# Optimization experiments

Hardware: AMD Instinct MI355X
Metric: run time of the kernel (lower is better)

## Reference

```python
import jax, jax.numpy as jnp
import numpy as np

POOL = 7  # fixed 7x7 output grid, hard-coded in the original layer


def _bin_bounds(step, rlen):
    # Replicates the original bin-corner logic + empty-bin adjustment.
    i = jnp.arange(POOL, dtype=jnp.int32)
    s = i * step
    e = jnp.where(i < POOL - 1, (i + 1) * step, rlen)
    empty = s == e
    # original: grow end by 1 if room, else shrink start by 1
    e = jnp.where(empty & (e < rlen), e + 1, e)
    s = jnp.where(empty & ~(e > (i * step)) , s, s)  # no-op placeholder for clarity
    s = jnp.where(empty & ((i * step) == e), (i * step) - 1, jnp.where(empty, i * step, s))
    # simpler equivalent: if still empty after trying to grow end, shrink start
    s0 = i * step
    e0 = jnp.where(i < POOL - 1, (i + 1) * step, rlen)
    grow = empty & (e0 < rlen)
    e = jnp.where(grow, e0 + 1, e0)
    s = jnp.where(empty & ~grow, s0 - 1, s0)
    return s, e


def _pool_one(roi, fm):
    # fm: [H, W, C]; roi: [4] normalized (y1, x1, y2, x2)
    H, W, C = fm.shape
    h0 = (H * roi[0]).astype(jnp.int32)  # tf.cast to int32 truncates (floor for >=0)
    w0 = (W * roi[1]).astype(jnp.int32)
    h1 = (H * roi[2]).astype(jnp.int32)
    w1 = (W * roi[3]).astype(jnp.int32)
    rh = h1 - h0
    rw = w1 - w0
    hstep = rh // POOL
    wstep = rw // POOL
    sh, eh = _bin_bounds(hstep, rh)  # [7], region-relative
    sw, ew = _bin_bounds(wstep, rw)
    hidx = jnp.arange(H, dtype=jnp.int32)
    widx = jnp.arange(W, dtype=jnp.int32)
    rmask = (hidx[None, :] >= (h0 + sh)[:, None]) & (hidx[None, :] < (h0 + eh)[:, None])  # [7,H]
    cmask = (widx[None, :] >= (w0 + sw)[:, None]) & (widx[None, :] < (w0 + ew)[:, None])  # [7,W]
    neg = jnp.asarray(-jnp.inf, fm.dtype)
    # max over rows for each of the 7 row-bins: [7, W, C]
    t = jnp.max(jnp.where(rmask[:, :, None, None], fm[None, :, :, :], neg), axis=1)
    # max over cols for each of the 7 col-bins: [7, 7, C]
    out = jnp.max(jnp.where(cmask[None, :, :, None], t[:, None, :, :], neg), axis=2)
    return out


def setup_inputs() -> dict:
    key = jax.random.key(0)
    k_f, k_y, k_x, k_h, k_w = jax.random.split(key, 5)
    H, W, C, N = 50, 50, 1024, 300
    features = jax.random.normal(k_f, (1, H, W, C), dtype=jnp.float32)
    # well-formed normalized ROIs: y1 < y2, x1 < x2, extent in [0.2, 0.55]
    y1 = jax.random.uniform(k_y, (N,), minval=0.0, maxval=0.45)
    x1 = jax.random.uniform(k_x, (N,), minval=0.0, maxval=0.45)
    hh = jax.random.uniform(k_h, (N,), minval=0.2, maxval=0.55)
    ww = jax.random.uniform(k_w, (N,), minval=0.2, maxval=0.55)
    rois = jnp.stack([y1, x1, jnp.minimum(y1 + hh, 1.0), jnp.minimum(x1 + ww, 1.0)], axis=1).astype(jnp.float32)
    return {"features": features, "rois": rois}


def reference(features, rois):
    fm = jnp.squeeze(features, axis=0)  # [H, W, C]
    # sequential over ROIs (mirrors tf.while_loop), fully vectorized per ROI
    pooled = jax.lax.map(lambda r: _pool_one(r, fm), rois)  # [N, 7, 7, C]
    return pooled
```

## Files before the change

### kernel.cpp

```cpp
#include <hip/hip_runtime.h>
#include <math.h>

#define POOL 7
#define FH 50
#define FW 50
#define FC 1024
#define FC4 (FC / 4)
#define CHUNKS 4
#define F4C 64
#define RS (FW * FC4)
#define JGROUPS 4
#define UNITS_PER_ROI (POOL * JGROUPS)
#define GRID 1024

typedef float vf4 __attribute__((ext_vector_type(4)));

static __device__ __forceinline__ vf4 vmax4(vf4 a, vf4 b) {
    vf4 r;
    r.x = fmaxf(a.x, b.x);
    r.y = fmaxf(a.y, b.y);
    r.z = fmaxf(a.z, b.z);
    r.w = fmaxf(a.w, b.w);
    return r;
}

template<int W>
static __device__ __forceinline__ void pool_w(
    const vf4* __restrict__ base,
    int r0, int nrows, int w0, int rw, int jg,
    vf4& a0, vf4& a1)
{
    if (jg < 3) {
        const int c0 = w0 + (jg * 2) * W;
        const vf4* p = base + (size_t)r0 * RS + (size_t)c0 * FC4;
        int t = 0;
        for (; t + 2 <= nrows; t += 2) {
            vf4 v0[2 * W], v1[2 * W];
#pragma unroll
            for (int k = 0; k < 2 * W; ++k) v0[k] = p[k * FC4];
#pragma unroll
            for (int k = 0; k < 2 * W; ++k) v1[k] = p[RS + k * FC4];
#pragma unroll
            for (int k = 0; k < W; ++k) a0 = vmax4(a0, vmax4(v0[k], v1[k]));
#pragma unroll
            for (int k = W; k < 2 * W; ++k) a1 = vmax4(a1, vmax4(v0[k], v1[k]));
            p += 2 * RS;
        }
        if (t < nrows) {
            vf4 v0[2 * W];
#pragma unroll
            for (int k = 0; k < 2 * W; ++k) v0[k] = p[k * FC4];
#pragma unroll
            for (int k = 0; k < W; ++k) a0 = vmax4(a0, v0[k]);
#pragma unroll
            for (int k = W; k < 2 * W; ++k) a1 = vmax4(a1, v0[k]);
        }
    } else {
        const int bw = rw - 6 * W;
        const int c0 = w0 + 6 * W;
        const vf4* p = base + (size_t)r0 * RS + (size_t)c0 * FC4;
        for (int r = 0; r < nrows; ++r) {
            vf4 v[W + 6];
#pragma unroll
            for (int k = 0; k < W + 6; ++k) {
                const int kc = (k < bw) ? k : (bw - 1);
                v[k] = p[kc * FC4];
            }
#pragma unroll
            for (int k = 0; k < W + 6; ++k) a0 = vmax4(a0, v[k]);
            p += RS;
        }
    }
}

__global__ __launch_bounds__(256, 4) void roipool_kernel(
    const float* __restrict__ fm,
    const float* __restrict__ rois,
    float* __restrict__ out,
    int nunits)
{
    const int b     = blockIdx.x;
    const int chunk = b & (CHUNKS - 1);
    const int wave  = threadIdx.x >> 6;
    const int lane  = threadIdx.x & 63;
    const int wv    = (b >> 2) * 4 + wave;

    const int f4 = chunk * F4C + lane;
    const vf4* base = reinterpret_cast<const vf4*>(fm) + f4;

    for (int u = wv; u < nunits; u += GRID) {
        const int n   = u / UNITS_PER_ROI;
        const int rem = u - n * UNITS_PER_ROI;
        const int i   = rem >> 2;
        const int jg  = rem & 3;
        const int j0  = jg * 2;
        const int jcnt = (jg < JGROUPS - 1) ? 2 : 1;

        const float4 roi = reinterpret_cast<const float4*>(rois)[n];
        const int h0 = (int)((float)FH * roi.x);
        const int w0 = (int)((float)FW * roi.y);
        const int h1 = (int)((float)FH * roi.z);
        const int w1 = (int)((float)FW * roi.w);
        const int rh = h1 - h0;
        const int rw = w1 - w0;
        const int hstep = rh / POOL;
        const int wstep = rw / POOL;

        vf4 a0 = {-INFINITY, -INFINITY, -INFINITY, -INFINITY};
        vf4 a1 = a0;

        if (hstep >= 1 && wstep >= 1 && wstep <= 3) {
            const int r0    = h0 + i * hstep;
            const int nrows = (i < POOL - 1) ? hstep : (rh - 6 * hstep);
            switch (wstep) {
                case 1: pool_w<1>(base, r0, nrows, w0, rw, jg, a0, a1); break;
                case 2: pool_w<2>(base, r0, nrows, w0, rw, jg, a0, a1); break;
                default: pool_w<3>(base, r0, nrows, w0, rw, jg, a0, a1); break;
            }
        } else {
            int sh = i * hstep;
            int eh = (i < POOL - 1) ? (i + 1) * hstep : rh;
            if (sh == eh) { if (eh < rh) eh += 1; else sh -= 1; }
            const int rr0 = max(0, h0 + sh);
            const int rr1 = min(FH, h0 + eh);

            int c0[2], c1[2];
#pragma unroll
            for (int t = 0; t < 2; ++t) {
                const int j = j0 + t;
                if (j < POOL) {
                    int sw = j * wstep;
                    int ew = (j < POOL - 1) ? (j + 1) * wstep : rw;
                    if (sw == ew) { if (ew < rw) ew += 1; else sw -= 1; }
                    c0[t] = max(0, w0 + sw);
                    c1[t] = min(FW, w0 + ew);
                } else {
                    c0[t] = 0; c1[t] = 0;
                }
            }
            for (int r = rr0; r < rr1; ++r) {
                const vf4* rowp = base + (size_t)r * RS;
#pragma unroll
                for (int t = 0; t < 2; ++t) {
                    vf4 acc = (t == 0) ? a0 : a1;
                    for (int c = c0[t]; c < c1[t]; ++c) {
                        acc = vmax4(acc, rowp[c * FC4]);
                    }
                    if (t == 0) a0 = acc; else a1 = acc;
                }
            }
        }

        vf4* o = reinterpret_cast<vf4*>(out)
               + (size_t)(n * 49 + i * 7 + j0) * FC4 + f4;
        __builtin_nontemporal_store(a0, o);
        if (jcnt == 2) {
            __builtin_nontemporal_store(a1, o + (size_t)FC4);
        }
    }
}

extern "C" void kernel_launch(void* const* d_in, const int* in_sizes, int n_in,
                              void* d_out, int out_size, void* d_ws, size_t ws_size,
                              hipStream_t stream) {
    const float* features = (const float*)d_in[0];
    const float* rois     = (const float*)d_in[1];
    float* out            = (float*)d_out;
    const int N = in_sizes[1] / 4;

    const int nunits = N * UNITS_PER_ROI;
    dim3 grid(GRID);
    dim3 block(256);
    roipool_kernel<<<grid, block, 0, stream>>>(features, rois, out, nunits);
}
```

Baseline: 102.7 us.

## Precompute 2x2/2x1/1x2 max tables to cut per-bin load count

Adds a prepass kernel that builds pairwise-max tables (vertical pair, horizontal pair, 2x2 quad) of the feature map in workspace. The pooling kernel then covers each bin with overlapping 2-strided reads from these tables, roughly halving or quartering the number of loads per bin. The cost is an extra kernel launch that reads the full feature map and writes up to three map-sized tables. The templated unrolled per-wstep paths are replaced by a generic loop.

```diff
diff --git a/kernel.cpp b/kernel.cpp
--- a/kernel.cpp
+++ b/kernel.cpp
@@ -12,6 +12,9 @@
 #define JGROUPS 4
 #define UNITS_PER_ROI (POOL * JGROUPS)
 #define GRID 1024
+#define NCELLS (FH * FW)
+#define TBL_ELEMS ((size_t)NCELLS * FC)
+#define TBL_BYTES (TBL_ELEMS * sizeof(float))
 
 typedef float vf4 __attribute__((ext_vector_type(4)));
 
@@ -24,60 +27,37 @@
     return r;
 }
 
-template<int W>
-static __device__ __forceinline__ void pool_w(
-    const vf4* __restrict__ base,
-    int r0, int nrows, int w0, int rw, int jg,
-    vf4& a0, vf4& a1)
+__global__ __launch_bounds__(256) void build_tables(
+    const float* __restrict__ fm,
+    float* __restrict__ p1, float* __restrict__ c1, float* __restrict__ q,
+    int mask)
 {
-    if (jg < 3) {
-        const int c0 = w0 + (jg * 2) * W;
-        const vf4* p = base + (size_t)r0 * RS + (size_t)c0 * FC4;
-        int t = 0;
-        for (; t + 2 <= nrows; t += 2) {
-            vf4 v0[2 * W], v1[2 * W];
-#pragma unroll
-            for (int k = 0; k < 2 * W; ++k) v0[k] = p[k * FC4];
-#pragma unroll
-            for (int k = 0; k < 2 * W; ++k) v1[k] = p[RS + k * FC4];
-#pragma unroll
-            for (int k = 0; k < W; ++k) a0 = vmax4(a0, vmax4(v0[k], v1[k]));
-#pragma unroll
-            for (int k = W; k < 2 * W; ++k) a1 = vmax4(a1, vmax4(v0[k], v1[k]));
-            p += 2 * RS;
-        }
-        if (t < nrows) {
-            vf4 v0[2 * W];
-#pragma unroll
-            for (int k = 0; k < 2 * W; ++k) v0[k] = p[k * FC4];
-#pragma unroll
-            for (int k = 0; k < W; ++k) a0 = vmax4(a0, v0[k]);
-#pragma unroll
-            for (int k = W; k < 2 * W; ++k) a1 = vmax4(a1, v0[k]);
-        }
-    } else {
-        const int bw = rw - 6 * W;
-        const int c0 = w0 + 6 * W;
-        const vf4* p = base + (size_t)r0 * RS + (size_t)c0 * FC4;
-        for (int r = 0; r < nrows; ++r) {
-            vf4 v[W + 6];
-#pragma unroll
-            for (int k = 0; k < W + 6; ++k) {
-                const int kc = (k < bw) ? k : (bw - 1);
-                v[k] = p[kc * FC4];
-            }
-#pragma unroll
-            for (int k = 0; k < W + 6; ++k) a0 = vmax4(a0, v[k]);
-            p += RS;
-        }
-    }
+    const int cell = blockIdx.x;
+    const int t    = threadIdx.x;
+    const int r    = cell / FW;
+    const int c    = cell - r * FW;
+    const int rr   = (r + 1 < FH) ? r + 1 : r;
+    const int cc   = (c + 1 < FW) ? c + 1 : c;
+
+    const vf4* fm4 = reinterpret_cast<const vf4*>(fm);
+    const size_t i00 = (size_t)cell * FC4 + t;
+    const vf4 v00 = fm4[(size_t)(r  * FW + c ) * FC4 + t];
+    const vf4 v10 = fm4[(size_t)(rr * FW + c ) * FC4 + t];
+    const vf4 v01 = fm4[(size_t)(r  * FW + cc) * FC4 + t];
+    const vf4 v11 = fm4[(size_t)(rr * FW + cc) * FC4 + t];
+
+    if (mask & 1) reinterpret_cast<vf4*>(p1)[i00] = vmax4(v00, v10);
+    if (mask & 2) reinterpret_cast<vf4*>(c1)[i00] = vmax4(v00, v01);
+    if (mask & 4) reinterpret_cast<vf4*>(q)[i00]  = vmax4(vmax4(v00, v10), vmax4(v01, v11));
 }
 
 __global__ __launch_bounds__(256, 4) void roipool_kernel(
     const float* __restrict__ fm,
     const float* __restrict__ rois,
     float* __restrict__ out,
-    int nunits)
+    int nunits,
+    const float* __restrict__ p1, const float* __restrict__ c1,
+    const float* __restrict__ q, int mask)
 {
     const int b     = blockIdx.x;
     const int chunk = b & (CHUNKS - 1);
@@ -86,7 +66,6 @@
     const int wv    = (b >> 2) * 4 + wave;
 
     const int f4 = chunk * F4C + lane;
-    const vf4* base = reinterpret_cast<const vf4*>(fm) + f4;
 
     for (int u = wv; u < nunits; u += GRID) {
         const int n   = u / UNITS_PER_ROI;
@@ -106,16 +85,44 @@
         const int hstep = rh / POOL;
         const int wstep = rw / POOL;
 
-        vf4 a0 = {-INFINITY, -INFINITY, -INFINITY, -INFINITY};
-        vf4 a1 = a0;
+        vf4* o = reinterpret_cast<vf4*>(out)
+               + (size_t)(n * 49 + i * 7 + j0) * FC4 + f4;
 
-        if (hstep >= 1 && wstep >= 1 && wstep <= 3) {
-            const int r0    = h0 + i * hstep;
-            const int nrows = (i < POOL - 1) ? hstep : (rh - 6 * hstep);
-            switch (wstep) {
-                case 1: pool_w<1>(base, r0, nrows, w0, rw, jg, a0, a1); break;
-                case 2: pool_w<2>(base, r0, nrows, w0, rw, jg, a0, a1); break;
-                default: pool_w<3>(base, r0, nrows, w0, rw, jg, a0, a1); break;
+        if (hstep >= 1 && wstep >= 1) {
+            const int row0 = h0 + i * hstep;
+            const int hr   = (i < POOL - 1) ? hstep : (rh - 6 * hstep);
+            for (int t = 0; t < jcnt; ++t) {
+                const int j    = j0 + t;
+                const int wc   = (j < POOL - 1) ? wstep : (rw - 6 * wstep);
+                const int col0 = w0 + j * wstep;
+
+                const float* tb; int sr, sc;
+                if (hr >= 2 && wc >= 2 && (mask & 4))      { tb = q;  sr = 2; sc = 2; }
+                else if (hr == 1 && wc >= 2 && (mask & 2)) { tb = c1; sr = 1; sc = 2; }
+                else if (wc == 1 && hr >= 2 && (mask & 1)) { tb = p1; sr = 2; sc = 1; }
+                else                                       { tb = fm; sr = 1; sc = 1; }
+                const int rn = (sr == 2) ? ((hr + 1) >> 1) : hr;
+                const int cn = (sc == 2) ? ((wc + 1) >> 1) : wc;
+
+                const vf4* tb4 = reinterpret_cast<const vf4*>(tb) + f4;
+                vf4 acc = {-INFINITY, -INFINITY, -INFINITY, -INFINITY};
+                for (int a = 0; a < rn; ++a) {
+                    const int ro = (sr == 2) ? min(2 * a, hr - 2) : a;
+                    const vf4* rowp = tb4 + (size_t)(row0 + ro) * RS;
+                    int bb = 0;
+                    for (; bb + 2 <= cn; bb += 2) {
+                        const int co0 = (sc == 2) ? min(2 * bb, wc - 2) : bb;
+                        const int co1 = (sc == 2) ? min(2 * (bb + 1), wc - 2) : (bb + 1);
+                        vf4 x = rowp[(size_t)(col0 + co0) * FC4];
+                        vf4 y = rowp[(size_t)(col0 + co1) * FC4];
+                        acc = vmax4(acc, vmax4(x, y));
+                    }
+                    if (bb < cn) {
+                        const int co = (sc == 2) ? min(2 * bb, wc - 2) : bb;
+                        acc = vmax4(acc, rowp[(size_t)(col0 + co) * FC4]);
+                    }
+                }
+                __builtin_nontemporal_store(acc, o + (size_t)t * FC4);
             }
         } else {
             int sh = i * hstep;
@@ -124,7 +131,7 @@
             const int rr0 = max(0, h0 + sh);
             const int rr1 = min(FH, h0 + eh);
 
-            int c0[2], c1[2];
+            int c0[2], c1b[2];
 #pragma unroll
             for (int t = 0; t < 2; ++t) {
                 const int j = j0 + t;
@@ -132,30 +139,30 @@
                     int sw = j * wstep;
                     int ew = (j < POOL - 1) ? (j + 1) * wstep : rw;
                     if (sw == ew) { if (ew < rw) ew += 1; else sw -= 1; }
-                    c0[t] = max(0, w0 + sw);
-                    c1[t] = min(FW, w0 + ew);
+                    c0[t]  = max(0, w0 + sw);
+                    c1b[t] = min(FW, w0 + ew);
                 } else {
-                    c0[t] = 0; c1[t] = 0;
+                    c0[t] = 0; c1b[t] = 0;
                 }
             }
+            vf4 a0 = {-INFINITY, -INFINITY, -INFINITY, -INFINITY};
+            vf4 a1 = a0;
+            const vf4* base = reinterpret_cast<const vf4*>(fm) + f4;
             for (int r = rr0; r < rr1; ++r) {
                 const vf4* rowp = base + (size_t)r * RS;
 #pragma unroll
                 for (int t = 0; t < 2; ++t) {
                     vf4 acc = (t == 0) ? a0 : a1;
-                    for (int c = c0[t]; c < c1[t]; ++c) {
+                    for (int c = c0[t]; c < c1b[t]; ++c) {
                         acc = vmax4(acc, rowp[c * FC4]);
                     }
                     if (t == 0) a0 = acc; else a1 = acc;
                 }
             }
-        }
-
-        vf4* o = reinterpret_cast<vf4*>(out)
-               + (size_t)(n * 49 + i * 7 + j0) * FC4 + f4;
-        __builtin_nontemporal_store(a0, o);
-        if (jcnt == 2) {
-            __builtin_nontemporal_store(a1, o + (size_t)FC4);
+            __builtin_nontemporal_store(a0, o);
+            if (jcnt == 2) {
+                __builtin_nontemporal_store(a1, o + (size_t)FC4);
+            }
         }
     }
 }
@@ -167,9 +174,21 @@
     const float* rois     = (const float*)d_in[1];
     float* out            = (float*)d_out;
     const int N = in_sizes[1] / 4;
+    const int nunits = N * UNITS_PER_ROI;
 
-    const int nunits = N * UNITS_PER_ROI;
-    dim3 grid(GRID);
+    int mask = 0;
+    float *p1 = nullptr, *c1 = nullptr, *q = nullptr;
+    float* ws = (float*)d_ws;
+    if (ws_size >= 3 * TBL_BYTES) {
+        p1 = ws; c1 = ws + TBL_ELEMS; q = ws + 2 * TBL_ELEMS; mask = 7;
+    } else if (ws_size >= TBL_BYTES) {
+        q = ws; mask = 4;
+    }
+
     dim3 block(256);
-    roipool_kernel<<<grid, block, 0, stream>>>(features, rois, out, nunits);
+    if (mask) {
+        build_tables<<<dim3(NCELLS), block, 0, stream>>>(features, p1, c1, q, mask);
+    }
+    roipool_kernel<<<dim3(GRID), block, 0, stream>>>(features, rois, out, nunits,
+                                                     p1, c1, q, mask);
 }
```

Measured after the change: 101.5 us. No clear change (-1.1%).

## Flatten bin cells into batches of eight inline-asm loads per bin

Applied to the files above, without the earlier changes.

Replaces the templated per-width row loops with a generic routine that walks each bin's cells as a flat index. It issues them in batches of eight global_load_dwordx4 instructions from inline asm, each batch followed by a full vmcnt wait. Each of the two bins in a unit is now processed separately, and the occupancy hint in launch_bounds is dropped. The aim is a uniform number of loads in flight regardless of bin shape, but the full wait per batch serialises memory latency and repeated clamped addresses make redundant loads on partial batches.

```diff
diff --git a/kernel.cpp b/kernel.cpp
--- a/kernel.cpp
+++ b/kernel.cpp
@@ -24,56 +24,48 @@
     return r;
 }
 
-template<int W>
-static __device__ __forceinline__ void pool_w(
-    const vf4* __restrict__ base,
-    int r0, int nrows, int w0, int rw, int jg,
-    vf4& a0, vf4& a1)
+static __device__ __forceinline__ vf4 pool_bin8(const vf4* p0, int hr, int wd)
 {
-    if (jg < 3) {
-        const int c0 = w0 + (jg * 2) * W;
-        const vf4* p = base + (size_t)r0 * RS + (size_t)c0 * FC4;
-        int t = 0;
-        for (; t + 2 <= nrows; t += 2) {
-            vf4 v0[2 * W], v1[2 * W];
+    vf4 acc = {-INFINITY, -INFINITY, -INFINITY, -INFINITY};
+    const int cells = hr * wd;
+    const int nb = (cells + 7) >> 3;
+    const vf4* p = p0;
+    int co = 0;
+    for (int bk = 0; bk < nb; ++bk) {
+        const vf4* ap[8];
 #pragma unroll
-            for (int k = 0; k < 2 * W; ++k) v0[k] = p[k * FC4];
-#pragma unroll
-            for (int k = 0; k < 2 * W; ++k) v1[k] = p[RS + k * FC4];
-#pragma unroll
-            for (int k = 0; k < W; ++k) a0 = vmax4(a0, vmax4(v0[k], v1[k]));
-#pragma unroll
-            for (int k = W; k < 2 * W; ++k) a1 = vmax4(a1, vmax4(v0[k], v1[k]));
-            p += 2 * RS;
+        for (int k = 0; k < 8; ++k) {
+            ap[k] = p;
+            const bool adv  = (bk * 8 + k) < (cells - 1);
+            const int  con  = co + 1;
+            const bool wrap = (con == wd);
+            const vf4* pn   = wrap ? (p + (RS - (wd - 1) * FC4)) : (p + FC4);
+            p  = adv ? pn : p;
+            co = adv ? (wrap ? 0 : con) : co;
         }
-        if (t < nrows) {
-            vf4 v0[2 * W];
-#pragma unroll
-            for (int k = 0; k < 2 * W; ++k) v0[k] = p[k * FC4];
-#pragma unroll
-            for (int k = 0; k < W; ++k) a0 = vmax4(a0, v0[k]);
-#pragma unroll
-            for (int k = W; k < 2 * W; ++k) a1 = vmax4(a1, v0[k]);
-        }
-    } else {
-        const int bw = rw - 6 * W;
-        const int c0 = w0 + 6 * W;
-        const vf4* p = base + (size_t)r0 * RS + (size_t)c0 * FC4;
-        for (int r = 0; r < nrows; ++r) {
-            vf4 v[W + 6];
-#pragma unroll
-            for (int k = 0; k < W + 6; ++k) {
-                const int kc = (k < bw) ? k : (bw - 1);
-                v[k] = p[kc * FC4];
-            }
-#pragma unroll
-            for (int k = 0; k < W + 6; ++k) a0 = vmax4(a0, v[k]);
-            p += RS;
-        }
+        vf4 d0, d1, d2, d3, d4, d5, d6, d7;
+        asm volatile(
+            "global_load_dwordx4 %0, %8, off\n\t"
+            "global_load_dwordx4 %1, %9, off\n\t"
+            "global_load_dwordx4 %2, %10, off\n\t"
+            "global_load_dwordx4 %3, %11, off\n\t"
+            "global_load_dwordx4 %4, %12, off\n\t"
+            "global_load_dwordx4 %5, %13, off\n\t"
+            "global_load_dwordx4 %6, %14, off\n\t"
+            "global_load_dwordx4 %7, %15, off\n\t"
+            "s_waitcnt vmcnt(0)"
+            : "=&v"(d0), "=&v"(d1), "=&v"(d2), "=&v"(d3),
+              "=&v"(d4), "=&v"(d5), "=&v"(d6), "=&v"(d7)
+            : "v"(ap[0]), "v"(ap[1]), "v"(ap[2]), "v"(ap[3]),
+              "v"(ap[4]), "v"(ap[5]), "v"(ap[6]), "v"(ap[7])
+            : "memory");
+        acc = vmax4(acc, vmax4(vmax4(d0, d1), vmax4(d2, d3)));
+        acc = vmax4(acc, vmax4(vmax4(d4, d5), vmax4(d6, d7)));
     }
+    return acc;
 }
 
-__global__ __launch_bounds__(256, 4) void roipool_kernel(
+__global__ __launch_bounds__(256) void roipool_kernel(
     const float* __restrict__ fm,
     const float* __restrict__ rois,
     float* __restrict__ out,
@@ -106,16 +98,24 @@
         const int hstep = rh / POOL;
         const int wstep = rw / POOL;
 
-        vf4 a0 = {-INFINITY, -INFINITY, -INFINITY, -INFINITY};
-        vf4 a1 = a0;
+        vf4* o = reinterpret_cast<vf4*>(out)
+               + (size_t)(n * 49 + i * 7 + j0) * FC4 + f4;
 
         if (hstep >= 1 && wstep >= 1 && wstep <= 3) {
-            const int r0    = h0 + i * hstep;
-            const int nrows = (i < POOL - 1) ? hstep : (rh - 6 * hstep);
-            switch (wstep) {
-                case 1: pool_w<1>(base, r0, nrows, w0, rw, jg, a0, a1); break;
-                case 2: pool_w<2>(base, r0, nrows, w0, rw, jg, a0, a1); break;
-                default: pool_w<3>(base, r0, nrows, w0, rw, jg, a0, a1); break;
+            const int row0 = h0 + i * hstep;
+            const int hr   = (i < POOL - 1) ? hstep : (rh - 6 * hstep);
+            {
+                const int wd   = (jg < 3) ? wstep : (rw - 6 * wstep);
+                const int colb = w0 + j0 * wstep;
+                const vf4* p0  = base + (size_t)row0 * RS + (size_t)colb * FC4;
+                vf4 a0 = pool_bin8(p0, hr, wd);
+                __builtin_nontemporal_store(a0, o);
+            }
+            if (jcnt == 2) {
+                const int colb = w0 + (j0 + 1) * wstep;
+                const vf4* p0  = base + (size_t)row0 * RS + (size_t)colb * FC4;
+                vf4 a1 = pool_bin8(p0, hr, wstep);
+                __builtin_nontemporal_store(a1, o + (size_t)FC4);
             }
         } else {
             int sh = i * hstep;
@@ -138,6 +138,8 @@
                     c0[t] = 0; c1[t] = 0;
                 }
             }
+            vf4 a0 = {-INFINITY, -INFINITY, -INFINITY, -INFINITY};
+            vf4 a1 = a0;
             for (int r = rr0; r < rr1; ++r) {
                 const vf4* rowp = base + (size_t)r * RS;
 #pragma unroll
@@ -149,13 +151,10 @@
                     if (t == 0) a0 = acc; else a1 = acc;
                 }
             }
-        }
-
-        vf4* o = reinterpret_cast<vf4*>(out)
-               + (size_t)(n * 49 + i * 7 + j0) * FC4 + f4;
-        __builtin_nontemporal_store(a0, o);
-        if (jcnt == 2) {
-            __builtin_nontemporal_store(a1, o + (size_t)FC4);
+            __builtin_nontemporal_store(a0, o);
+            if (jcnt == 2) {
+                __builtin_nontemporal_store(a1, o + (size_t)FC4);
+            }
         }
     }
 }
```

Result: slower. 107.9 us (+5.1%).
